# Kernel tuning notes

Measured on AMD Instinct MI355X. Metric: run time of the kernel, lower is better.

The kernel has to match this reference:

```python
import jax, jax.numpy as jnp
import numpy as np

N = 50000   # num_nodes
E = 250000  # edges per view
D = 128     # in_dim = h_dim = out_dim
B = 4       # num_bases
RELS = (8, 12, 6)


def setup_inputs() -> dict:
    key = jax.random.key(0)
    ks = iter(jax.random.split(key, 64))
    s = 1.0 / np.sqrt(D)
    inp = {"node_features": jax.random.normal(next(ks), (N, D), jnp.float32) * 0.1}
    for v, R in enumerate(RELS, start=1):
        inp[f"src{v}"] = jax.random.randint(next(ks), (E,), 0, N)
        inp[f"dst{v}"] = jax.random.randint(next(ks), (E,), 0, N)
        inp[f"rel{v}"] = jax.random.randint(next(ks), (E,), 0, R)
        for l in (1, 2):
            inp[f"v{v}_bases{l}"] = jax.random.normal(next(ks), (B, D, D), jnp.float32) * s
            inp[f"v{v}_coef{l}"] = jax.random.normal(next(ks), (R, B), jnp.float32) * 0.5
            inp[f"v{v}_loopw{l}"] = jax.random.normal(next(ks), (D, D), jnp.float32) * s
            inp[f"v{v}_bias{l}"] = jnp.zeros((D,), jnp.float32)
    inp["fusion_w"] = jax.random.normal(next(ks), (3 * D, D), jnp.float32) * (1.0 / np.sqrt(3 * D))
    inp["fusion_b"] = jnp.zeros((D,), jnp.float32)
    return inp


def rgcn_layer(h, src, dst, rel, bases, coef, loop_w, bias, act):
    # basis trick: project nodes through all bases once, then combine per edge
    node_proj = jnp.einsum('ni,bio->nbo', h, bases)          # [N,B,out]
    msg = jnp.einsum('eb,ebo->eo', coef[rel], node_proj[src])  # [E,out]
    agg = jax.ops.segment_sum(msg, dst, num_segments=h.shape[0])
    out = agg + h @ loop_w + bias                             # self-loop + bias (DGL defaults)
    return jax.nn.relu(out) if act else out


def single_view(feats, src, dst, rel, bases1, coef1, loopw1, bias1,
                bases2, coef2, loopw2, bias2):
    h = rgcn_layer(feats, src, dst, rel, bases1, coef1, loopw1, bias1, act=True)
    return rgcn_layer(h, src, dst, rel, bases2, coef2, loopw2, bias2, act=False)


def reference(node_features,
              src1, dst1, rel1, src2, dst2, rel2, src3, dst3, rel3,
              v1_bases1, v1_coef1, v1_loopw1, v1_bias1,
              v1_bases2, v1_coef2, v1_loopw2, v1_bias2,
              v2_bases1, v2_coef1, v2_loopw1, v2_bias1,
              v2_bases2, v2_coef2, v2_loopw2, v2_bias2,
              v3_bases1, v3_coef1, v3_loopw1, v3_bias1,
              v3_bases2, v3_coef2, v3_loopw2, v3_bias2,
              fusion_w, fusion_b):
    h1 = single_view(node_features, src1, dst1, rel1,
                     v1_bases1, v1_coef1, v1_loopw1, v1_bias1,
                     v1_bases2, v1_coef2, v1_loopw2, v1_bias2)
    h2 = single_view(node_features, src2, dst2, rel2,
                     v2_bases1, v2_coef1, v2_loopw1, v2_bias1,
                     v2_bases2, v2_coef2, v2_loopw2, v2_bias2)
    h3 = single_view(node_features, src3, dst3, rel3,
                     v3_bases1, v3_coef1, v3_loopw1, v3_bias1,
                     v3_bases2, v3_coef2, v3_loopw2, v3_bias2)
    h_cat = jnp.concatenate([h1, h2, h3], axis=-1)  # [N, 3*D]
    return h_cat @ fusion_w + fusion_b
```

## Files before the change

kernel.cpp:

```cpp
#include <hip/hip_runtime.h>
#include <hip/hip_bf16.h>
#include <stdint.h>

typedef _Float16 f16x8 __attribute__((ext_vector_type(8)));
typedef _Float16 f16x2 __attribute__((ext_vector_type(2)));
typedef float f32x4 __attribute__((ext_vector_type(4)));


__device__ __forceinline__ void gll16(const _Float16* g, _Float16* l) {
    __builtin_amdgcn_global_load_lds(
        (const __attribute__((address_space(1))) void*)g,
        (__attribute__((address_space(3))) void*)l, 16, 0, 0);
}

struct PrepDesc { const float* src; _Float16* dst; int dstride; };
struct PrepArgs { PrepDesc d[33]; };

__global__ __launch_bounds__(256) void prep_weights(PrepArgs args) {
    __shared__ _Float16 lds[128 * 129];
    const PrepDesc de = args.d[blockIdx.x];
    int t = threadIdx.x;
    for (int q = 0; q < 64; ++q) {
        int li = t + q * 256;
        int i = li >> 7, o = li & 127;
        lds[o * 129 + i] = (_Float16)de.src[li];
    }
    __syncthreads();
    for (int q = 0; q < 64; ++q) {
        int lo = t + q * 256;
        int o = lo >> 7, i = lo & 127;
        de.dst[(size_t)o * de.dstride + (i ^ ((o & 7) << 3))] = lds[o * 129 + i];
    }
}

__global__ __launch_bounds__(256) void f32_to_f16(const float* __restrict__ in,
                                                  _Float16* __restrict__ out, int n4) {
    int i = blockIdx.x * 256 + threadIdx.x;
    if (i >= n4) return;
    float4 v = *((const float4*)in + i);
    int n = i >> 5;
    int c = (i & 31) * 4;
    int cs = c ^ ((n & 7) << 3);
    f16x2 a, b;
    a[0] = (_Float16)v.x; a[1] = (_Float16)v.y;
    b[0] = (_Float16)v.z; b[1] = (_Float16)v.w;
    _Float16* o = out + (size_t)n * 128 + cs;
    *(f16x2*)o = a;
    *(f16x2*)(o + 2) = b;
}

struct EdgeArgs {
    const int* src[3]; const int* dst[3]; const int* rel[3];
    int E[3]; int N;
};

__global__ __launch_bounds__(256) void zero_deg(int* __restrict__ deg3, int n) {
    int i = blockIdx.x * 256 + threadIdx.x;
    if (i < n) deg3[i] = 0;
}

__global__ __launch_bounds__(256) void hist3(EdgeArgs ea, int* __restrict__ deg3) {
    int v = blockIdx.y;
    const int* dst = ea.dst[v];
    int* deg = deg3 + (size_t)v * ea.N;
    for (int e = blockIdx.x * 256 + threadIdx.x; e < ea.E[v]; e += gridDim.x * 256)
        atomicAdd(&deg[dst[e]], 1);
}

__global__ __launch_bounds__(256) void scan1_kernel(const int* __restrict__ deg,
                                                    int* __restrict__ off,
                                                    int* __restrict__ bsum, int n) {
    __shared__ int s[256];
    int b = blockIdx.x, t = threadIdx.x;
    int base = b * 2048 + t * 8;
    int v[8]; int sum = 0;
    for (int j = 0; j < 8; ++j) {
        int x = (base + j < n) ? deg[base + j] : 0;
        v[j] = sum;
        sum += x;
    }
    s[t] = sum;
    __syncthreads();
    for (int st = 1; st < 256; st <<= 1) {
        int y = (t >= st) ? s[t - st] : 0;
        __syncthreads();
        s[t] += y;
        __syncthreads();
    }
    int texcl = t ? s[t - 1] : 0;
    if (t == 255) bsum[b] = s[255];
    for (int j = 0; j < 8; ++j)
        if (base + j < n) off[base + j] = texcl + v[j];
}

__global__ __launch_bounds__(256) void scan2_kernel(int* __restrict__ off,
                                                    int* __restrict__ cur,
                                                    const int* __restrict__ bsum,
                                                    int n, int Etot) {
    __shared__ int pref;
    int b = blockIdx.x, t = threadIdx.x;
    if (t == 0) { int p = 0; for (int j = 0; j < b; ++j) p += bsum[j]; pref = p; }
    __syncthreads();
    int p = pref;
    int base = b * 2048 + t * 8;
    for (int j = 0; j < 8; ++j)
        if (base + j < n) { int x = off[base + j] + p; off[base + j] = x; cur[base + j] = x; }
    if (b == 0 && t == 0) off[n] = Etot;
}

__global__ __launch_bounds__(256) void scatter3(EdgeArgs ea, int* __restrict__ cur3,
                                                int* __restrict__ packed3) {
    int v = blockIdx.y;
    const int* src = ea.src[v];
    const int* dst = ea.dst[v];
    const int* rel = ea.rel[v];
    int* cur = cur3 + (size_t)v * ea.N;
    for (int e = blockIdx.x * 256 + threadIdx.x; e < ea.E[v]; e += gridDim.x * 256) {
        int pos = atomicAdd(&cur[dst[e]], 1);
        packed3[pos] = src[e] | (rel[e] << 20);
    }
}

struct GatherArgs {
    const int* off3;
    const int* packed3;
    const float* coef[3];
    const _Float16* h[3];
    _Float16* T;
    int N; size_t Tvs;
};

__global__ __launch_bounds__(256) void gather3(GatherArgs g) {
    int v = blockIdx.y;
    int node = (blockIdx.x << 2) | (threadIdx.x >> 6);
    if (node >= g.N) return;
    int lane = threadIdx.x & 63;
    const int* off = g.off3 + (size_t)v * g.N;
    const float* coef = g.coef[v];
    const _Float16* h = g.h[v];
    _Float16* T = g.T + (size_t)v * g.Tvs;

    int i  = __builtin_amdgcn_readfirstlane(off[node]);
    int e1 = __builtin_amdgcn_readfirstlane(off[node + 1]);
    float acc[8] = {};

    for (; i + 3 < e1; i += 4) {
        int p0 = __builtin_amdgcn_readfirstlane(g.packed3[i]);
        int p1 = __builtin_amdgcn_readfirstlane(g.packed3[i + 1]);
        int p2 = __builtin_amdgcn_readfirstlane(g.packed3[i + 2]);
        int p3 = __builtin_amdgcn_readfirstlane(g.packed3[i + 3]);
        int s0 = p0 & 0xFFFFF, r0 = p0 >> 20;
        int s1 = p1 & 0xFFFFF, r1 = p1 >> 20;
        int s2 = p2 & 0xFFFFF, r2 = p2 >> 20;
        int s3 = p3 & 0xFFFFF, r3 = p3 >> 20;
        uint32_t q0 = ((const uint32_t*)(h + (size_t)s0 * 128))[lane ^ ((s0 & 7) << 2)];
        uint32_t q1 = ((const uint32_t*)(h + (size_t)s1 * 128))[lane ^ ((s1 & 7) << 2)];
        uint32_t q2 = ((const uint32_t*)(h + (size_t)s2 * 128))[lane ^ ((s2 & 7) << 2)];
        uint32_t q3 = ((const uint32_t*)(h + (size_t)s3 * 128))[lane ^ ((s3 & 7) << 2)];
        float4 c0 = *(const float4*)(coef + (size_t)r0 * 4);
        float4 c1 = *(const float4*)(coef + (size_t)r1 * 4);
        float4 c2 = *(const float4*)(coef + (size_t)r2 * 4);
        float4 c3 = *(const float4*)(coef + (size_t)r3 * 4);
        f16x2 u0 = __builtin_bit_cast(f16x2, q0);
        f16x2 u1 = __builtin_bit_cast(f16x2, q1);
        f16x2 u2 = __builtin_bit_cast(f16x2, q2);
        f16x2 u3 = __builtin_bit_cast(f16x2, q3);
        float lo0 = (float)u0[0], hi0 = (float)u0[1];
        float lo1 = (float)u1[0], hi1 = (float)u1[1];
        float lo2 = (float)u2[0], hi2 = (float)u2[1];
        float lo3 = (float)u3[0], hi3 = (float)u3[1];
        acc[0] += c0.x * lo0 + c1.x * lo1 + c2.x * lo2 + c3.x * lo3;
        acc[1] += c0.x * hi0 + c1.x * hi1 + c2.x * hi2 + c3.x * hi3;
        acc[2] += c0.y * lo0 + c1.y * lo1 + c2.y * lo2 + c3.y * lo3;
        acc[3] += c0.y * hi0 + c1.y * hi1 + c2.y * hi2 + c3.y * hi3;
        acc[4] += c0.z * lo0 + c1.z * lo1 + c2.z * lo2 + c3.z * lo3;
        acc[5] += c0.z * hi0 + c1.z * hi1 + c2.z * hi2 + c3.z * hi3;
        acc[6] += c0.w * lo0 + c1.w * lo1 + c2.w * lo2 + c3.w * lo3;
        acc[7] += c0.w * hi0 + c1.w * hi1 + c2.w * hi2 + c3.w * hi3;
    }
    for (; i < e1; ++i) {
        int p0 = __builtin_amdgcn_readfirstlane(g.packed3[i]);
        int s0 = p0 & 0xFFFFF, r0 = p0 >> 20;
        uint32_t q0 = ((const uint32_t*)(h + (size_t)s0 * 128))[lane ^ ((s0 & 7) << 2)];
        float4 c0 = *(const float4*)(coef + (size_t)r0 * 4);
        f16x2 u0 = __builtin_bit_cast(f16x2, q0);
        float lo0 = (float)u0[0], hi0 = (float)u0[1];
        acc[0] += c0.x * lo0;  acc[1] += c0.x * hi0;
        acc[2] += c0.y * lo0;  acc[3] += c0.y * hi0;
        acc[4] += c0.z * lo0;  acc[5] += c0.z * hi0;
        acc[6] += c0.w * lo0;  acc[7] += c0.w * hi0;
    }
    int cs = (2 * lane) ^ ((node & 7) << 3);
    _Float16* tb = T + (size_t)node * 512 + cs;
    for (int b = 0; b < 4; ++b) {
        f16x2 o; o[0] = (_Float16)acc[2 * b]; o[1] = (_Float16)acc[2 * b + 1];
        *(f16x2*)(tb + b * 128) = o;
    }
}

struct GemmArgs {
    const _Float16* T;
    const _Float16* hin[3];
    const _Float16* WT[3];
    const float* bias[3];
    _Float16* hout;
    int M; int relu; size_t Tvs; size_t hovs;
};

__global__ __launch_bounds__(512) void gemm_layer(GemmArgs ga) {
    __shared__ _Float16 As[64 * 128];
    __shared__ _Float16 Bs[128 * 128];
    int v = blockIdx.y;
    const _Float16* Tb  = ga.T + (size_t)v * ga.Tvs;
    const _Float16* hin = ga.hin[v];
    const _Float16* BT  = ga.WT[v];
    const float* bias   = ga.bias[v];
    _Float16* out       = ga.hout + (size_t)v * ga.hovs;
    int M = ga.M;

    int tid = threadIdx.x;
    int m0 = blockIdx.x * 64;
    int wid = tid >> 6, lane = tid & 63;
    int wr = (wid >> 2) * 32;
    int wc = (wid & 3) * 32;
    int lm = lane & 15;
    int lk = (lane >> 4) * 8;
    int xm = (lm & 7) << 3;

    f32x4 acc[2][2] = {};

    for (int kb = 0; kb < 5; ++kb) {
        const _Float16* Asrc; size_t astride;
        if (kb < 4) { Asrc = Tb + (size_t)kb * 128; astride = 512; }
        else        { Asrc = hin;                   astride = 128; }
        for (int q = 0; q < 2; ++q) {
            int li = tid + q * 512;
            int r = li >> 4;
            int c = (li & 15) << 3;
            int gr = m0 + r; if (gr >= M) gr = M - 1;
            gll16(Asrc + (size_t)gr * astride + c, As + (size_t)li * 8);
        }
        for (int q = 0; q < 4; ++q) {
            int li = tid + q * 512;
            gll16(BT + (size_t)(li >> 4) * 640 + kb * 128 + ((li & 15) << 3),
                  Bs + (size_t)li * 8);
        }
        __syncthreads();

        for (int ks = 0; ks < 4; ++ks) {
            int ac = (ks * 32 + lk) ^ xm;
            f16x8 a[2], b[2];
            for (int mi = 0; mi < 2; ++mi)
                a[mi] = *(const f16x8*)(As + (wr + mi * 16 + lm) * 128 + ac);
            for (int ni = 0; ni < 2; ++ni)
                b[ni] = *(const f16x8*)(Bs + (wc + ni * 16 + lm) * 128 + ac);
            for (int mi = 0; mi < 2; ++mi)
                for (int ni = 0; ni < 2; ++ni)
                    acc[mi][ni] = __builtin_amdgcn_mfma_f32_16x16x32_f16(a[mi], b[ni], acc[mi][ni], 0, 0, 0);
        }
        __syncthreads();
    }

    int rbase = (lane >> 4) * 4;
    for (int mi = 0; mi < 2; ++mi) {
        for (int j = 0; j < 4; ++j) {
            int gr = m0 + wr + mi * 16 + rbase + j;
            if (gr >= M) continue;
            int rs = (gr & 7) << 3;
            for (int ni = 0; ni < 2; ++ni) {
                int col = wc + ni * 16 + lm;
                float val = acc[mi][ni][j] + bias[col];
                if (ga.relu) val = fmaxf(val, 0.f);
                out[(size_t)gr * 128 + (col ^ rs)] = (_Float16)val;
            }
        }
    }
}

struct FusArgs {
    const _Float16* A[3];
    const _Float16* BT;
    const float* bias;
    float* out; int M;
};

__global__ __launch_bounds__(256) void gemm_fusion(FusArgs fa) {
    __shared__ _Float16 As[128 * 128];
    __shared__ _Float16 Bs[128 * 128];
    int tid = threadIdx.x;
    int m0 = blockIdx.x * 128;
    int M = fa.M;
    int wid = tid >> 6, lane = tid & 63;
    int wr = (wid >> 1) * 64;
    int wc = (wid & 1) * 64;
    int lm = lane & 15;
    int lk = (lane >> 4) * 8;
    int xm = (lm & 7) << 3;

    f32x4 acc[4][4] = {};

    for (int kb = 0; kb < 3; ++kb) {
        const _Float16* Asrc = fa.A[kb];
        for (int q = 0; q < 8; ++q) {
            int li = tid + q * 256;
            int r = li >> 4;
            int c = (li & 15) << 3;
            int gr = m0 + r; if (gr >= M) gr = M - 1;
            gll16(Asrc + (size_t)gr * 128 + c, As + (size_t)li * 8);
        }
        for (int q = 0; q < 8; ++q) {
            int li = tid + q * 256;
            gll16(fa.BT + (size_t)(li >> 4) * 384 + kb * 128 + ((li & 15) << 3),
                  Bs + (size_t)li * 8);
        }
        __syncthreads();

        for (int ks = 0; ks < 4; ++ks) {
            int ac = (ks * 32 + lk) ^ xm;
            f16x8 a[4], b[4];
            for (int mi = 0; mi < 4; ++mi)
                a[mi] = *(const f16x8*)(As + (wr + mi * 16 + lm) * 128 + ac);
            for (int ni = 0; ni < 4; ++ni)
                b[ni] = *(const f16x8*)(Bs + (wc + ni * 16 + lm) * 128 + ac);
            for (int mi = 0; mi < 4; ++mi)
                for (int ni = 0; ni < 4; ++ni)
                    acc[mi][ni] = __builtin_amdgcn_mfma_f32_16x16x32_f16(a[mi], b[ni], acc[mi][ni], 0, 0, 0);
        }
        __syncthreads();
    }

    int rbase = (lane >> 4) * 4;
    for (int mi = 0; mi < 4; ++mi) {
        for (int j = 0; j < 4; ++j) {
            int gr = m0 + wr + mi * 16 + rbase + j;
            if (gr >= M) continue;
            for (int ni = 0; ni < 4; ++ni) {
                int col = wc + ni * 16 + lm;
                fa.out[(size_t)gr * 128 + col] = acc[mi][ni][j] + fa.bias[col];
            }
        }
    }
}

extern "C" void kernel_launch(void* const* d_in, const int* in_sizes, int n_in,
                              void* d_out, int out_size, void* d_ws, size_t ws_size,
                              hipStream_t stream) {
    const int D = 128;
    const int M = in_sizes[0] / D;

    struct ViewIn {
        const int *src, *dst, *rel;
        const float *bases1, *coef1, *loopw1, *bias1;
        const float *bases2, *coef2, *loopw2, *bias2;
        int E;
    } V[3];
    int idx = 1;
    for (int v = 0; v < 3; ++v) {
        V[v].src    = (const int*)d_in[idx + 0];
        V[v].dst    = (const int*)d_in[idx + 1];
        V[v].rel    = (const int*)d_in[idx + 2];
        V[v].bases1 = (const float*)d_in[idx + 3];
        V[v].coef1  = (const float*)d_in[idx + 4];
        V[v].loopw1 = (const float*)d_in[idx + 5];
        V[v].bias1  = (const float*)d_in[idx + 6];
        V[v].bases2 = (const float*)d_in[idx + 7];
        V[v].coef2  = (const float*)d_in[idx + 8];
        V[v].loopw2 = (const float*)d_in[idx + 9];
        V[v].bias2  = (const float*)d_in[idx + 10];
        V[v].E      = in_sizes[idx + 0];
        idx += 11;
    }
    const float* fusion_w = (const float*)d_in[idx];
    const float* fusion_b = (const float*)d_in[idx + 1];
    int Etot = V[0].E + V[1].E + V[2].E;

    char* w = (char*)d_ws;
    auto alloc = [&](size_t bytes) -> char* {
        char* p = w; w += (bytes + 255) & ~(size_t)255; return p;
    };
    _Float16* nf16 = (_Float16*)alloc((size_t)M * 128 * 2);
    _Float16* wts  = (_Float16*)alloc((size_t)(6 * 81920 + 49152) * 2);
    int* deg3      = (int*)alloc((size_t)3 * M * 4);
    int* cur3      = (int*)alloc((size_t)3 * M * 4);
    int* bsum      = (int*)alloc(512);
    int* off3      = (int*)alloc(((size_t)3 * M + 1) * 4);
    int* packed3   = (int*)alloc((size_t)Etot * 4);
    _Float16* T3   = (_Float16*)alloc((size_t)3 * M * 512 * 2);
    _Float16* h1b  = (_Float16*)alloc((size_t)3 * M * 128 * 2);
    _Float16* h2b  = (_Float16*)alloc((size_t)3 * M * 128 * 2);

    _Float16 *WT[3][2];
    for (int v = 0; v < 3; ++v)
        for (int l = 0; l < 2; ++l)
            WT[v][l] = wts + (size_t)(v * 2 + l) * 81920;
    _Float16* fusTcat = wts + 6 * 81920;

    PrepArgs pa;
    int t = 0;
    for (int v = 0; v < 3; ++v) {
        const float* bases[2] = { V[v].bases1, V[v].bases2 };
        const float* loopw[2] = { V[v].loopw1, V[v].loopw2 };
        for (int l = 0; l < 2; ++l) {
            for (int b = 0; b < 4; ++b) {
                pa.d[t].src = bases[l] + (size_t)b * 16384;
                pa.d[t].dst = WT[v][l] + (size_t)b * 128;
                pa.d[t].dstride = 640; ++t;
            }
            pa.d[t].src = loopw[l];
            pa.d[t].dst = WT[v][l] + 512;
            pa.d[t].dstride = 640; ++t;
        }
    }
    for (int v = 0; v < 3; ++v) {
        pa.d[t].src = fusion_w + (size_t)v * 16384;
        pa.d[t].dst = fusTcat + (size_t)v * 128;
        pa.d[t].dstride = 384; ++t;
    }
    prep_weights<<<33, 256, 0, stream>>>(pa);

    int n4 = M * D / 4;
    f32_to_f16<<<(n4 + 255) / 256, 256, 0, stream>>>((const float*)d_in[0], nf16, n4);

    EdgeArgs ea;
    for (int v = 0; v < 3; ++v) {
        ea.src[v] = V[v].src; ea.dst[v] = V[v].dst; ea.rel[v] = V[v].rel; ea.E[v] = V[v].E;
    }
    ea.N = M;
    int n3 = 3 * M;
    zero_deg<<<(n3 + 255) / 256, 256, 0, stream>>>(deg3, n3);
    hist3<<<dim3(512, 3), 256, 0, stream>>>(ea, deg3);
    int nsb = (n3 + 2047) / 2048;
    scan1_kernel<<<nsb, 256, 0, stream>>>(deg3, off3, bsum, n3);
    scan2_kernel<<<nsb, 256, 0, stream>>>(off3, cur3, bsum, n3, Etot);
    scatter3<<<dim3(512, 3), 256, 0, stream>>>(ea, cur3, packed3);

    int ng  = (M + 3) / 4;
    int gxL = (M + 63) / 64;
    int gxF = (M + 127) / 128;
    size_t Tvs = (size_t)M * 512;
    size_t hvs = (size_t)M * 128;
    float* outF = (float*)d_out;

    GatherArgs g1;
    g1.off3 = off3; g1.packed3 = packed3; g1.T = T3; g1.N = M; g1.Tvs = Tvs;
    for (int v = 0; v < 3; ++v) { g1.coef[v] = V[v].coef1; g1.h[v] = nf16; }
    gather3<<<dim3(ng, 3), 256, 0, stream>>>(g1);

    GemmArgs m1;
    m1.T = T3; m1.hout = h1b; m1.M = M; m1.relu = 1; m1.Tvs = Tvs; m1.hovs = hvs;
    for (int v = 0; v < 3; ++v) { m1.hin[v] = nf16; m1.WT[v] = WT[v][0]; m1.bias[v] = V[v].bias1; }
    gemm_layer<<<dim3(gxL, 3), 512, 0, stream>>>(m1);

    GatherArgs g2 = g1;
    for (int v = 0; v < 3; ++v) { g2.coef[v] = V[v].coef2; g2.h[v] = h1b + (size_t)v * hvs; }
    gather3<<<dim3(ng, 3), 256, 0, stream>>>(g2);

    GemmArgs m2;
    m2.T = T3; m2.hout = h2b; m2.M = M; m2.relu = 0; m2.Tvs = Tvs; m2.hovs = hvs;
    for (int v = 0; v < 3; ++v) { m2.hin[v] = h1b + (size_t)v * hvs; m2.WT[v] = WT[v][1]; m2.bias[v] = V[v].bias2; }
    gemm_layer<<<dim3(gxL, 3), 512, 0, stream>>>(m2);

    FusArgs fa;
    for (int v = 0; v < 3; ++v) fa.A[v] = h2b + (size_t)v * hvs;
    fa.BT = fusTcat; fa.bias = fusion_b; fa.out = outF; fa.M = M;
    gemm_fusion<<<gxF, 256, 0, stream>>>(fa);
}
```

Measured before the change: 331.7 us.

## Build CSR with two-pass bucketed radix sort using LDS atomics

Replaces the global-atomic degree histogram and scatter with a two-level bucket sort. Edges are first binned by dst>>8 using per-block LDS histograms and scattered to an intermediate array. A per-bucket kernel then sorts by the low 8 bits of dst and writes the offsets and packed edges. The aim is to avoid contended global atomics and the zero/degree passes, at the cost of an extra pass over the edges and an extra buffer; src must now fit in 16 bits.

After: 288.9 us. -12.9%, faster.

```diff
diff --git a/kernel.cpp b/kernel.cpp
--- a/kernel.cpp
+++ b/kernel.cpp
@@ -54,17 +54,21 @@
     int E[3]; int N;
 };
 
-__global__ __launch_bounds__(256) void zero_deg(int* __restrict__ deg3, int n) {
-    int i = blockIdx.x * 256 + threadIdx.x;
-    if (i < n) deg3[i] = 0;
-}
-
-__global__ __launch_bounds__(256) void hist3(EdgeArgs ea, int* __restrict__ deg3) {
-    int v = blockIdx.y;
+__global__ __launch_bounds__(256) void bhist(EdgeArgs ea, int* __restrict__ hmat, int nbk) {
+    __shared__ int cnt[256];
+    int v = blockIdx.y, blk = blockIdx.x, t = threadIdx.x;
+    cnt[t] = 0;
+    __syncthreads();
+    int E = ea.E[v];
     const int* dst = ea.dst[v];
-    int* deg = deg3 + (size_t)v * ea.N;
-    for (int e = blockIdx.x * 256 + threadIdx.x; e < ea.E[v]; e += gridDim.x * 256)
-        atomicAdd(&deg[dst[e]], 1);
+    int chunk = (E + 63) >> 6;
+    int e0 = blk * chunk;
+    int e1 = min(e0 + chunk, E);
+    for (int e = e0 + t; e < e1; e += 256)
+        atomicAdd(&cnt[dst[e] >> 8], 1);
+    __syncthreads();
+    if (t < nbk)
+        hmat[((size_t)v * nbk + t) * 64 + blk] = cnt[t];
 }
 
 __global__ __launch_bounds__(256) void scan1_kernel(const int* __restrict__ deg,
@@ -93,10 +97,9 @@
         if (base + j < n) off[base + j] = texcl + v[j];
 }
 
-__global__ __launch_bounds__(256) void scan2_kernel(int* __restrict__ off,
-                                                    int* __restrict__ cur,
-                                                    const int* __restrict__ bsum,
-                                                    int n, int Etot) {
+__global__ __launch_bounds__(256) void scan2b(int* __restrict__ off,
+                                              const int* __restrict__ bsum,
+                                              int n, int Etot) {
     __shared__ int pref;
     int b = blockIdx.x, t = threadIdx.x;
     if (t == 0) { int p = 0; for (int j = 0; j < b; ++j) p += bsum[j]; pref = p; }
@@ -104,21 +107,66 @@
     int p = pref;
     int base = b * 2048 + t * 8;
     for (int j = 0; j < 8; ++j)
-        if (base + j < n) { int x = off[base + j] + p; off[base + j] = x; cur[base + j] = x; }
+        if (base + j < n) off[base + j] += p;
     if (b == 0 && t == 0) off[n] = Etot;
 }
 
-__global__ __launch_bounds__(256) void scatter3(EdgeArgs ea, int* __restrict__ cur3,
-                                                int* __restrict__ packed3) {
-    int v = blockIdx.y;
+__global__ __launch_bounds__(256) void bscat(EdgeArgs ea, const int* __restrict__ smat,
+                                             int* __restrict__ mid, int nbk) {
+    __shared__ int cur[256];
+    int v = blockIdx.y, blk = blockIdx.x, t = threadIdx.x;
+    if (t < nbk) cur[t] = smat[((size_t)v * nbk + t) * 64 + blk];
+    __syncthreads();
+    int E = ea.E[v];
     const int* src = ea.src[v];
     const int* dst = ea.dst[v];
     const int* rel = ea.rel[v];
-    int* cur = cur3 + (size_t)v * ea.N;
-    for (int e = blockIdx.x * 256 + threadIdx.x; e < ea.E[v]; e += gridDim.x * 256) {
-        int pos = atomicAdd(&cur[dst[e]], 1);
-        packed3[pos] = src[e] | (rel[e] << 20);
-    }
+    int chunk = (E + 63) >> 6;
+    int e0 = blk * chunk;
+    int e1 = min(e0 + chunk, E);
+    for (int e = e0 + t; e < e1; e += 256) {
+        int d = dst[e];
+        int pos = atomicAdd(&cur[d >> 8], 1);
+        mid[pos] = src[e] | (rel[e] << 16) | ((d & 255) << 20);
+    }
+}
+
+__global__ __launch_bounds__(256) void bfinal(const int* __restrict__ smat,
+                                              const int* __restrict__ mid,
+                                              int* __restrict__ off3,
+                                              int* __restrict__ packed3,
+                                              int M, int nbk, int Etot) {
+    __shared__ int cnt[256];
+    __shared__ int s[256];
+    __shared__ int cur[256];
+    int bk = blockIdx.x, v = blockIdx.y, t = threadIdx.x;
+    int flat0 = (v * nbk + bk) * 64;
+    int start = smat[flat0];
+    int end   = smat[flat0 + 64];
+    cnt[t] = 0;
+    __syncthreads();
+    for (int i = start + t; i < end; i += 256)
+        atomicAdd(&cnt[(mid[i] >> 20) & 255], 1);
+    __syncthreads();
+    s[t] = cnt[t];
+    __syncthreads();
+    for (int st = 1; st < 256; st <<= 1) {
+        int y = (t >= st) ? s[t - st] : 0;
+        __syncthreads();
+        s[t] += y;
+        __syncthreads();
+    }
+    int excl = t ? s[t - 1] : 0;
+    int node = (bk << 8) + t;
+    if (node < M) off3[(size_t)v * M + node] = start + excl;
+    cur[t] = start + excl;
+    __syncthreads();
+    for (int i = start + t; i < end; i += 256) {
+        int m = mid[i];
+        int pos = atomicAdd(&cur[(m >> 20) & 255], 1);
+        packed3[pos] = (m & 0xFFFF) | (((m >> 16) & 15) << 20);
+    }
+    if (v == 2 && bk == nbk - 1 && t == 0) off3[(size_t)3 * M] = Etot;
 }
 
 struct GatherArgs {
@@ -374,16 +422,20 @@
     const float* fusion_b = (const float*)d_in[idx + 1];
     int Etot = V[0].E + V[1].E + V[2].E;
 
+    int nbk = (M + 255) >> 8;
+    int nsc = 3 * nbk * 64;
+
     char* w = (char*)d_ws;
     auto alloc = [&](size_t bytes) -> char* {
         char* p = w; w += (bytes + 255) & ~(size_t)255; return p;
     };
     _Float16* nf16 = (_Float16*)alloc((size_t)M * 128 * 2);
     _Float16* wts  = (_Float16*)alloc((size_t)(6 * 81920 + 49152) * 2);
-    int* deg3      = (int*)alloc((size_t)3 * M * 4);
-    int* cur3      = (int*)alloc((size_t)3 * M * 4);
+    int* hmat      = (int*)alloc((size_t)nsc * 4);
+    int* smat      = (int*)alloc(((size_t)nsc + 1) * 4);
     int* bsum      = (int*)alloc(512);
     int* off3      = (int*)alloc(((size_t)3 * M + 1) * 4);
+    int* mid       = (int*)alloc((size_t)Etot * 4);
     int* packed3   = (int*)alloc((size_t)Etot * 4);
     _Float16* T3   = (_Float16*)alloc((size_t)3 * M * 512 * 2);
     _Float16* h1b  = (_Float16*)alloc((size_t)3 * M * 128 * 2);
@@ -426,13 +478,12 @@
         ea.src[v] = V[v].src; ea.dst[v] = V[v].dst; ea.rel[v] = V[v].rel; ea.E[v] = V[v].E;
     }
     ea.N = M;
-    int n3 = 3 * M;
-    zero_deg<<<(n3 + 255) / 256, 256, 0, stream>>>(deg3, n3);
-    hist3<<<dim3(512, 3), 256, 0, stream>>>(ea, deg3);
-    int nsb = (n3 + 2047) / 2048;
-    scan1_kernel<<<nsb, 256, 0, stream>>>(deg3, off3, bsum, n3);
-    scan2_kernel<<<nsb, 256, 0, stream>>>(off3, cur3, bsum, n3, Etot);
-    scatter3<<<dim3(512, 3), 256, 0, stream>>>(ea, cur3, packed3);
+    int nsb = (nsc + 2047) / 2048;
+    bhist<<<dim3(64, 3), 256, 0, stream>>>(ea, hmat, nbk);
+    scan1_kernel<<<nsb, 256, 0, stream>>>(hmat, smat, bsum, nsc);
+    scan2b<<<nsb, 256, 0, stream>>>(smat, bsum, nsc, Etot);
+    bscat<<<dim3(64, 3), 256, 0, stream>>>(ea, smat, mid, nbk);
+    bfinal<<<dim3(nbk, 3), 256, 0, stream>>>(smat, mid, off3, packed3, M, nbk, Etot);
 
     int ng  = (M + 3) / 4;
     int gxL = (M + 63) / 64;
```
